# Kernel tuning notes

Measured on AMD Instinct MI355X. Metric: run time of the kernel, lower is better.

The kernel has to match this reference:

```python
import jax, jax.numpy as jnp
import numpy as np

D = 256  # input_dim
B = 2048

def setup_inputs() -> dict:
    key = jax.random.key(0)
    ks = jax.random.split(key, 6)
    x = jax.random.normal(ks[0], (B, D), dtype=jnp.float32)
    offsets = jax.random.normal(ks[1], (D,), dtype=jnp.float32)
    coeff0 = jax.random.normal(ks[2], (), dtype=jnp.float32)
    coeff1 = jax.random.normal(ks[3], (D,), dtype=jnp.float32)
    coeff2 = jax.random.normal(ks[4], (D, D), dtype=jnp.float32)
    coeff3 = jax.random.normal(ks[5], (D, D, D), dtype=jnp.float32)
    return {"x": x, "offsets": offsets, "coeff0": coeff0, "coeff1": coeff1,
            "coeff2": coeff2, "coeff3": coeff3}

def reference(x, offsets, coeff0, coeff1, coeff2, coeff3):
    # Truncated Taylor series around learned offsets: out[b] = c0 + sum_i <coeff_i, rel^{\otimes i}>[b]
    rel = x - offsets  # (B, D)
    out = coeff0  # scalar, broadcasts to (B,)
    for c in (coeff1, coeff2, coeff3):
        # contract one mode of the rank-i coefficient with rel at a time
        t = jnp.einsum('...d,bd->b...', c, rel)  # (B, D^{i-1})
        while t.ndim > 1:
            t = jnp.einsum('b...d,bd->b...', t, rel)
        out = out + t  # (B,)
    return out
```

## Files before the change

### kernel.cpp

```cpp
#include <hip/hip_runtime.h>
#include <hip/hip_bf16.h>

#define DD 256
#define BB 2048
#define BM 128
#define BN 64
#define NTILE ((DD * DD) / BM)
#define NSTAGE (BB / BN)

typedef __bf16 bf16x8 __attribute__((ext_vector_type(8)));
typedef float  f32x4  __attribute__((ext_vector_type(4)));

#define AS1 __attribute__((address_space(1)))
#define AS3 __attribute__((address_space(3)))

__device__ __forceinline__ unsigned short f2bf(float f) {
    unsigned int u = __float_as_uint(f);
    return (unsigned short)((u + 0x7FFFu + ((u >> 16) & 1u)) >> 16);
}
__device__ __forceinline__ float bf2f(unsigned short s) {
    return __uint_as_float(((unsigned int)s) << 16);
}
__device__ __forceinline__ void async_cp16(const void* g, void* l) {
    __builtin_amdgcn_global_load_lds((const AS1 unsigned int*)g,
                                     (AS3 unsigned int*)l, 16, 0, 0);
}

__global__ void prep_rel(const float* __restrict__ x, const float* __restrict__ offsets,
                         float* __restrict__ rel_f32, unsigned short* __restrict__ rel_bf16) {
    int idx = blockIdx.x * 256 + threadIdx.x;
    int d = idx & (DD - 1);
    float r = x[idx] - offsets[d];
    rel_f32[idx] = r;
    rel_bf16[idx] = f2bf(r);
}

__global__ void init_out(const float* __restrict__ rel_f32, const float* __restrict__ c1,
                         const float* __restrict__ c0, float* __restrict__ out) {
    int b = blockIdx.x * 256 + threadIdx.x;
    const float4* rp = (const float4*)(rel_f32 + (size_t)b * DD);
    const float4* cp = (const float4*)c1;
    float s = c0[0];
#pragma unroll 8
    for (int i = 0; i < DD / 4; ++i) {
        float4 r = rp[i]; float4 c = cp[i];
        s += r.x * c.x + r.y * c.y + r.z * c.z + r.w * c.w;
    }
    out[b] = s;
}

__global__ __launch_bounds__(256, 2) void taylor3(
    const float* __restrict__ c3, const float* __restrict__ c2,
    const float* __restrict__ rel_f32, const unsigned short* __restrict__ rel_bf16,
    float* __restrict__ partial)
{
    __shared__ unsigned short Bs[2][BN * DD];

    const int tile = blockIdx.x;
    const int i_t   = tile >> 1;
    const int jbase = (tile & 1) << 7;
    const int tid  = threadIdx.x;
    const int wave = tid >> 6;
    const int lane = tid & 63;
    const int wm = wave & 1, wn = wave >> 1;
    const int lrow = lane & 15, quad = lane >> 4;

    bf16x8 afr[8][4];
    {
        const float* abase = c3 + (size_t)tile * BM * DD;
#pragma unroll
        for (int mt = 0; mt < 4; ++mt) {
            const int row = wm * 64 + mt * 16 + lrow;
            const float* p = abase + (size_t)row * DD + quad * 8;
#pragma unroll
            for (int ks = 0; ks < 8; ++ks) {
                float4 f0 = *(const float4*)(p + ks * 32);
                float4 f1 = *(const float4*)(p + ks * 32 + 4);
                union { unsigned short u[8]; bf16x8 v; } cv;
                cv.u[0] = f2bf(f0.x); cv.u[1] = f2bf(f0.y);
                cv.u[2] = f2bf(f0.z); cv.u[3] = f2bf(f0.w);
                cv.u[4] = f2bf(f1.x); cv.u[5] = f2bf(f1.y);
                cv.u[6] = f2bf(f1.z); cv.u[7] = f2bf(f1.w);
                afr[ks][mt] = cv.v;
            }
        }
    }
    float c2v[4][4];
#pragma unroll
    for (int mt = 0; mt < 4; ++mt)
#pragma unroll
        for (int r = 0; r < 4; ++r)
            c2v[mt][r] = c2[i_t * DD + jbase + wm * 64 + mt * 16 + quad * 4 + r];

    auto stage = [&](int nb, int buf) {
        const int b0 = nb * BN;
#pragma unroll
        for (int c = 0; c < 8; ++c) {
            const int r0 = wave * 16 + c * 2;
            const int row = r0 + (lane >> 5);
            const int g = (lane & 31) ^ (row & 7);
            const unsigned short* src = rel_bf16 + (size_t)(b0 + row) * DD + g * 8;
            async_cp16(src, &Bs[buf][r0 * DD]);
        }
    };

    stage(0, 0);

    for (int nb = 0; nb < NSTAGE; ++nb) {
        const int cur = nb & 1;
        const int b0 = nb * BN;
        __syncthreads();
        if (nb + 1 < NSTAGE) stage(nb + 1, cur ^ 1);

        f32x4 acc[4][2];
#pragma unroll
        for (int mt = 0; mt < 4; ++mt)
#pragma unroll
            for (int nt = 0; nt < 2; ++nt)
                acc[mt][nt] = (f32x4){0.f, 0.f, 0.f, 0.f};

#pragma unroll
        for (int ks = 0; ks < 8; ++ks) {
            bf16x8 bfr[2];
#pragma unroll
            for (int nt = 0; nt < 2; ++nt) {
                const int col = wn * 32 + nt * 16 + lrow;
                const int g = (ks * 4 + quad) ^ (col & 7);
                bfr[nt] = *(const bf16x8*)(&Bs[cur][col * DD + g * 8]);
            }
#pragma unroll
            for (int mt = 0; mt < 4; ++mt)
#pragma unroll
                for (int nt = 0; nt < 2; ++nt)
                    acc[mt][nt] = __builtin_amdgcn_mfma_f32_16x16x32_bf16(
                        afr[ks][mt], bfr[nt], acc[mt][nt], 0, 0, 0);
        }

        float sv[2];
#pragma unroll
        for (int nt = 0; nt < 2; ++nt) {
            const int col = wn * 32 + nt * 16 + lrow;
            float s = 0.f;
#pragma unroll
            for (int mt = 0; mt < 4; ++mt) {
                const int e = jbase + wm * 64 + mt * 16 + quad * 4;
                const int g = (e >> 3) ^ (col & 7);
                const ushort4 rj = *(const ushort4*)(&Bs[cur][col * DD + g * 8 + (e & 7)]);
                s += (acc[mt][nt][0] + c2v[mt][0]) * bf2f(rj.x);
                s += (acc[mt][nt][1] + c2v[mt][1]) * bf2f(rj.y);
                s += (acc[mt][nt][2] + c2v[mt][2]) * bf2f(rj.z);
                s += (acc[mt][nt][3] + c2v[mt][3]) * bf2f(rj.w);
            }
            s += __shfl_xor(s, 16, 64);
            s += __shfl_xor(s, 32, 64);
            sv[nt] = s;
        }
        if (lane < 32) {
            const int colS = wn * 32 + lane;
            const float relI = rel_f32[(size_t)(b0 + colS) * DD + i_t];
            partial[(size_t)(tile * 2 + wm) * BB + b0 + colS] = relI * sv[lane >> 4];
        }
    }
}

__global__ void reduce_partial(const float* __restrict__ partial, float* __restrict__ out) {
    __shared__ float4 red[256];
    const int t = threadIdx.x;
    const int g4 = blockIdx.x * 32 + (t & 31);
    const int rs = t >> 5;
    float4 s = {0.f, 0.f, 0.f, 0.f};
    for (int r = rs * 128; r < rs * 128 + 128; ++r) {
        float4 v = *(const float4*)(partial + (size_t)r * BB + g4 * 4);
        s.x += v.x; s.y += v.y; s.z += v.z; s.w += v.w;
    }
    red[t] = s; __syncthreads();
    if (t < 128) { float4 o = red[t + 128]; red[t].x += o.x; red[t].y += o.y; red[t].z += o.z; red[t].w += o.w; }
    __syncthreads();
    if (t < 64)  { float4 o = red[t + 64];  red[t].x += o.x; red[t].y += o.y; red[t].z += o.z; red[t].w += o.w; }
    __syncthreads();
    if (t < 32) {
        float4 a = red[t]; float4 b = red[t + 32];
        float4* op = (float4*)(out + (size_t)g4 * 4);
        float4 o = *op;
        o.x += a.x + b.x; o.y += a.y + b.y; o.z += a.z + b.z; o.w += a.w + b.w;
        *op = o;
    }
}

extern "C" void kernel_launch(void* const* d_in, const int* in_sizes, int n_in,
                              void* d_out, int out_size, void* d_ws, size_t ws_size,
                              hipStream_t stream) {
    const float* x       = (const float*)d_in[0];
    const float* offsets = (const float*)d_in[1];
    const float* c0      = (const float*)d_in[2];
    const float* c1      = (const float*)d_in[3];
    const float* c2      = (const float*)d_in[4];
    const float* c3      = (const float*)d_in[5];
    float* out = (float*)d_out;

    char* ws = (char*)d_ws;
    float* rel_f32 = (float*)ws;
    unsigned short* rel_bf16 = (unsigned short*)(ws + (size_t)BB * DD * 4);
    float* partial = (float*)(ws + (size_t)BB * DD * 6);

    prep_rel<<<(BB * DD) / 256, 256, 0, stream>>>(x, offsets, rel_f32, rel_bf16);
    init_out<<<BB / 256, 256, 0, stream>>>(rel_f32, c1, c0, out);
    taylor3<<<NTILE, 256, 0, stream>>>(c3, c2, rel_f32, rel_bf16, partial);
    reduce_partial<<<16, 256, 0, stream>>>(partial, out);
}
```

Before: 234.5 us.

## Widen taylor3 to 8 waves, reduce columns in LDS, fuse prep kernels

Each taylor3 block now runs 512 threads (8 waves), with each wave holding half as many A fragments. The four wm partial column sums are combined in shared memory before one write per tile, which cuts the partial buffer from 1024 to 512 rows. The rel_i values are preloaded into LDS, and each stage's writeback is deferred into the next iteration. prep_rel and init_out are fused into one kernel, and the reduction is regridded to 64 blocks. The gain is more waves to hide latency and less partial traffic, at the cost of more LDS per block, which could limit occupancy.

New measurement: 221.7 us. -5.4%, faster.

```diff
diff --git a/kernel.cpp b/kernel.cpp
--- a/kernel.cpp
+++ b/kernel.cpp
@@ -26,35 +26,38 @@
                                      (AS3 unsigned int*)l, 16, 0, 0);
 }
 
-__global__ void prep_rel(const float* __restrict__ x, const float* __restrict__ offsets,
-                         float* __restrict__ rel_f32, unsigned short* __restrict__ rel_bf16) {
-    int idx = blockIdx.x * 256 + threadIdx.x;
-    int d = idx & (DD - 1);
-    float r = x[idx] - offsets[d];
-    rel_f32[idx] = r;
-    rel_bf16[idx] = f2bf(r);
-}
-
-__global__ void init_out(const float* __restrict__ rel_f32, const float* __restrict__ c1,
-                         const float* __restrict__ c0, float* __restrict__ out) {
-    int b = blockIdx.x * 256 + threadIdx.x;
-    const float4* rp = (const float4*)(rel_f32 + (size_t)b * DD);
-    const float4* cp = (const float4*)c1;
-    float s = c0[0];
-#pragma unroll 8
-    for (int i = 0; i < DD / 4; ++i) {
-        float4 r = rp[i]; float4 c = cp[i];
-        s += r.x * c.x + r.y * c.y + r.z * c.z + r.w * c.w;
-    }
-    out[b] = s;
-}
-
-__global__ __launch_bounds__(256, 2) void taylor3(
+__global__ void prep_all(const float* __restrict__ x, const float* __restrict__ offsets,
+                         const float* __restrict__ c0, const float* __restrict__ c1,
+                         float* __restrict__ rel_f32, unsigned short* __restrict__ rel_bf16,
+                         float* __restrict__ out) {
+    const int tid = threadIdx.x, wave = tid >> 6, lane = tid & 63;
+    const float4 o4  = *(const float4*)(offsets + lane * 4);
+    const float4 c14 = *(const float4*)(c1 + lane * 4);
+#pragma unroll
+    for (int i = 0; i < 2; ++i) {
+        const int b = blockIdx.x * 8 + wave * 2 + i;
+        const float4 x4 = *(const float4*)(x + (size_t)b * DD + lane * 4);
+        float4 r;
+        r.x = x4.x - o4.x; r.y = x4.y - o4.y; r.z = x4.z - o4.z; r.w = x4.w - o4.w;
+        *(float4*)(rel_f32 + (size_t)b * DD + lane * 4) = r;
+        ushort4 rb;
+        rb.x = f2bf(r.x); rb.y = f2bf(r.y); rb.z = f2bf(r.z); rb.w = f2bf(r.w);
+        *(ushort4*)(rel_bf16 + (size_t)b * DD + lane * 4) = rb;
+        float s = r.x * c14.x + r.y * c14.y + r.z * c14.z + r.w * c14.w;
+        s += __shfl_xor(s, 1);  s += __shfl_xor(s, 2);  s += __shfl_xor(s, 4);
+        s += __shfl_xor(s, 8);  s += __shfl_xor(s, 16); s += __shfl_xor(s, 32);
+        if (lane == 0) out[b] = c0[0] + s;
+    }
+}
+
+__global__ __launch_bounds__(512, 4) void taylor3(
     const float* __restrict__ c3, const float* __restrict__ c2,
     const float* __restrict__ rel_f32, const unsigned short* __restrict__ rel_bf16,
     float* __restrict__ partial)
 {
     __shared__ unsigned short Bs[2][BN * DD];
+    __shared__ float relI[BB];
+    __shared__ float colsum[2][4][BN];
 
     const int tile = blockIdx.x;
     const int i_t   = tile >> 1;
@@ -62,15 +65,21 @@
     const int tid  = threadIdx.x;
     const int wave = tid >> 6;
     const int lane = tid & 63;
-    const int wm = wave & 1, wn = wave >> 1;
+    const int wm = wave & 3, wn = wave >> 2;
     const int lrow = lane & 15, quad = lane >> 4;
 
-    bf16x8 afr[8][4];
+#pragma unroll
+    for (int k = 0; k < 4; ++k) {
+        const int b = tid + k * 512;
+        relI[b] = rel_f32[(size_t)b * DD + i_t];
+    }
+
+    bf16x8 afr[8][2];
     {
         const float* abase = c3 + (size_t)tile * BM * DD;
 #pragma unroll
-        for (int mt = 0; mt < 4; ++mt) {
-            const int row = wm * 64 + mt * 16 + lrow;
+        for (int mt = 0; mt < 2; ++mt) {
+            const int row = wm * 32 + mt * 16 + lrow;
             const float* p = abase + (size_t)row * DD + quad * 8;
 #pragma unroll
             for (int ks = 0; ks < 8; ++ks) {
@@ -85,18 +94,18 @@
             }
         }
     }
-    float c2v[4][4];
-#pragma unroll
-    for (int mt = 0; mt < 4; ++mt)
+    float c2v[2][4];
+#pragma unroll
+    for (int mt = 0; mt < 2; ++mt)
 #pragma unroll
         for (int r = 0; r < 4; ++r)
-            c2v[mt][r] = c2[i_t * DD + jbase + wm * 64 + mt * 16 + quad * 4 + r];
+            c2v[mt][r] = c2[i_t * DD + jbase + wm * 32 + mt * 16 + quad * 4 + r];
 
     auto stage = [&](int nb, int buf) {
         const int b0 = nb * BN;
 #pragma unroll
-        for (int c = 0; c < 8; ++c) {
-            const int r0 = wave * 16 + c * 2;
+        for (int c = 0; c < 4; ++c) {
+            const int r0 = c * 16 + wave * 2;
             const int row = r0 + (lane >> 5);
             const int g = (lane & 31) ^ (row & 7);
             const unsigned short* src = rel_bf16 + (size_t)(b0 + row) * DD + g * 8;
@@ -105,6 +114,7 @@
     };
 
     stage(0, 0);
+    int prev_b0 = -1;
 
     for (int nb = 0; nb < NSTAGE; ++nb) {
         const int cur = nb & 1;
@@ -112,9 +122,15 @@
         __syncthreads();
         if (nb + 1 < NSTAGE) stage(nb + 1, cur ^ 1);
 
-        f32x4 acc[4][2];
-#pragma unroll
-        for (int mt = 0; mt < 4; ++mt)
+        if (prev_b0 >= 0 && tid < BN) {
+            const float v = colsum[cur ^ 1][0][tid] + colsum[cur ^ 1][1][tid]
+                          + colsum[cur ^ 1][2][tid] + colsum[cur ^ 1][3][tid];
+            partial[(size_t)tile * BB + prev_b0 + tid] = relI[prev_b0 + tid] * v;
+        }
+
+        f32x4 acc[2][2];
+#pragma unroll
+        for (int mt = 0; mt < 2; ++mt)
 #pragma unroll
             for (int nt = 0; nt < 2; ++nt)
                 acc[mt][nt] = (f32x4){0.f, 0.f, 0.f, 0.f};
@@ -129,7 +145,7 @@
                 bfr[nt] = *(const bf16x8*)(&Bs[cur][col * DD + g * 8]);
             }
 #pragma unroll
-            for (int mt = 0; mt < 4; ++mt)
+            for (int mt = 0; mt < 2; ++mt)
 #pragma unroll
                 for (int nt = 0; nt < 2; ++nt)
                     acc[mt][nt] = __builtin_amdgcn_mfma_f32_16x16x32_bf16(
@@ -142,8 +158,8 @@
             const int col = wn * 32 + nt * 16 + lrow;
             float s = 0.f;
 #pragma unroll
-            for (int mt = 0; mt < 4; ++mt) {
-                const int e = jbase + wm * 64 + mt * 16 + quad * 4;
+            for (int mt = 0; mt < 2; ++mt) {
+                const int e = jbase + wm * 32 + mt * 16 + quad * 4;
                 const int g = (e >> 3) ^ (col & 7);
                 const ushort4 rj = *(const ushort4*)(&Bs[cur][col * DD + g * 8 + (e & 7)]);
                 s += (acc[mt][nt][0] + c2v[mt][0]) * bf2f(rj.x);
@@ -155,34 +171,35 @@
             s += __shfl_xor(s, 32, 64);
             sv[nt] = s;
         }
-        if (lane < 32) {
-            const int colS = wn * 32 + lane;
-            const float relI = rel_f32[(size_t)(b0 + colS) * DD + i_t];
-            partial[(size_t)(tile * 2 + wm) * BB + b0 + colS] = relI * sv[lane >> 4];
-        }
+        if (lane < 32) colsum[cur][wm][wn * 32 + lane] = sv[lane >> 4];
+        prev_b0 = b0;
+    }
+    __syncthreads();
+    if (tid < BN) {
+        const float v = colsum[1][0][tid] + colsum[1][1][tid]
+                      + colsum[1][2][tid] + colsum[1][3][tid];
+        partial[(size_t)tile * BB + prev_b0 + tid] = relI[prev_b0 + tid] * v;
     }
 }
 
 __global__ void reduce_partial(const float* __restrict__ partial, float* __restrict__ out) {
-    __shared__ float4 red[256];
+    __shared__ f32x4 red[256];
     const int t = threadIdx.x;
-    const int g4 = blockIdx.x * 32 + (t & 31);
-    const int rs = t >> 5;
-    float4 s = {0.f, 0.f, 0.f, 0.f};
-    for (int r = rs * 128; r < rs * 128 + 128; ++r) {
-        float4 v = *(const float4*)(partial + (size_t)r * BB + g4 * 4);
-        s.x += v.x; s.y += v.y; s.z += v.z; s.w += v.w;
-    }
+    const int g = blockIdx.x * 8 + (t & 7);
+    const int slice = t >> 3;
+    f32x4 s = (f32x4){0.f, 0.f, 0.f, 0.f};
+    for (int r = slice * 16; r < slice * 16 + 16; ++r)
+        s += *(const f32x4*)(partial + (size_t)r * BB + g * 4);
     red[t] = s; __syncthreads();
-    if (t < 128) { float4 o = red[t + 128]; red[t].x += o.x; red[t].y += o.y; red[t].z += o.z; red[t].w += o.w; }
-    __syncthreads();
-    if (t < 64)  { float4 o = red[t + 64];  red[t].x += o.x; red[t].y += o.y; red[t].z += o.z; red[t].w += o.w; }
-    __syncthreads();
-    if (t < 32) {
-        float4 a = red[t]; float4 b = red[t + 32];
-        float4* op = (float4*)(out + (size_t)g4 * 4);
+    if (t < 128) red[t] += red[t + 128]; __syncthreads();
+    if (t < 64)  red[t] += red[t + 64];  __syncthreads();
+    if (t < 32)  red[t] += red[t + 32];  __syncthreads();
+    if (t < 16)  red[t] += red[t + 16];  __syncthreads();
+    if (t < 8) {
+        const f32x4 v = red[t] + red[t + 8];
+        float4* op = (float4*)(out + (size_t)(blockIdx.x * 8 + t) * 4);
         float4 o = *op;
-        o.x += a.x + b.x; o.y += a.y + b.y; o.z += a.z + b.z; o.w += a.w + b.w;
+        o.x += v[0]; o.y += v[1]; o.z += v[2]; o.w += v[3];
         *op = o;
     }
 }
@@ -203,8 +220,7 @@
     unsigned short* rel_bf16 = (unsigned short*)(ws + (size_t)BB * DD * 4);
     float* partial = (float*)(ws + (size_t)BB * DD * 6);
 
-    prep_rel<<<(BB * DD) / 256, 256, 0, stream>>>(x, offsets, rel_f32, rel_bf16);
-    init_out<<<BB / 256, 256, 0, stream>>>(rel_f32, c1, c0, out);
-    taylor3<<<NTILE, 256, 0, stream>>>(c3, c2, rel_f32, rel_bf16, partial);
-    reduce_partial<<<16, 256, 0, stream>>>(partial, out);
-}
+    prep_all<<<BB / 8, 256, 0, stream>>>(x, offsets, c0, c1, rel_f32, rel_bf16, out);
+    taylor3<<<NTILE, 512, 0, stream>>>(c3, c2, rel_f32, rel_bf16, partial);
+    reduce_partial<<<64, 256, 0, stream>>>(partial, out);
+}
```
